# Optimization experiments

Hardware: AMD Instinct MI355X
Metric: run time of the kernel (lower is better)

Reference implementation:

```python
import jax, jax.numpy as jnp
import numpy as np

N_NODES = 50000

def setup_inputs() -> dict:
    key = jax.random.key(0)
    k1, k2, k3, k4, k5, k6 = jax.random.split(key, 6)
    T, D, N, E = 10000, 128, N_NODES, 800000
    impact = jax.random.normal(k1, (T, D), dtype=jnp.float32)
    W = jax.random.normal(k2, (D, D), dtype=jnp.float32)
    M = jax.random.normal(k3, (D, D), dtype=jnp.float32)
    node_ids = jax.random.randint(k4, (N,), 0, T, dtype=jnp.int64)
    neighbor_ids = jax.random.randint(k5, (E,), 0, T, dtype=jnp.int64)
    neighbor_segments = jnp.sort(jax.random.randint(k6, (E,), 0, N, dtype=jnp.int64))
    return {"impact": impact, "W": W, "M": M, "node_ids": node_ids,
            "neighbor_ids": neighbor_ids, "neighbor_segments": neighbor_segments}

def reference(impact, W, M, node_ids, neighbor_ids, neighbor_segments):
    # Per node i (type k_i): s_i = relu(W @ h[k_i] + sum_{j in N(i)} M @ h[type_j])
    # result = softmax(sum_i s_i) over the D feature axis.
    self_feats = impact[node_ids]                          # (N, D) gather
    neigh_feats = impact[neighbor_ids]                     # (E, D) gather
    neigh_sum = jax.ops.segment_sum(neigh_feats, neighbor_segments,
                                    num_segments=N_NODES)  # (N, D) scatter-add
    pre = self_feats @ W.T + neigh_sum @ M.T               # (N, D)
    result = jnp.sum(jax.nn.relu(pre), axis=0)             # (D,)
    return jax.nn.softmax(result, axis=0)
```

## Files before the change

### kernel.cpp

```cpp
#include <hip/hip_runtime.h>
#include <hip/hip_fp16.h>

#define DDIM 128
#define ACC_BLOCKS 2048
#define NWALK (ACC_BLOCKS * 4)
#define RED_BLOCKS 64

typedef unsigned int uint;
typedef unsigned short ushort;
typedef __attribute__((ext_vector_type(8))) short bf16x8;
typedef __attribute__((ext_vector_type(4))) float f32x4;

static __device__ __forceinline__ ushort f2bf(float x) {
    uint u = __float_as_uint(x);
    u += 0x7fffu + ((u >> 16) & 1u);
    return (ushort)(u >> 16);
}

static __device__ __forceinline__ bf16x8 load_frag8(const float* base) {
    const float4 p = *reinterpret_cast<const float4*>(base);
    const float4 q = *reinterpret_cast<const float4*>(base + 4);
    bf16x8 f;
    f[0] = (short)f2bf(p.x); f[1] = (short)f2bf(p.y);
    f[2] = (short)f2bf(p.z); f[3] = (short)f2bf(p.w);
    f[4] = (short)f2bf(q.x); f[5] = (short)f2bf(q.y);
    f[6] = (short)f2bf(q.z); f[7] = (short)f2bf(q.w);
    return f;
}

__global__ __launch_bounds__(256) void fat_prep_precompute(
    const float* __restrict__ impact,
    const float* __restrict__ W,
    const float* __restrict__ Mm,
    __half* __restrict__ WhH,
    __half* __restrict__ MhH,
    const int* __restrict__ segs,
    const int* __restrict__ node_ids,
    const int* __restrict__ neighbor_ids,
    int* __restrict__ items,
    int* __restrict__ wstart,
    int* __restrict__ done,
    int T, int N, int E, int PB, int whoff, int mhoff)
{
    if ((int)blockIdx.x >= PB) {
        const int x = ((int)blockIdx.x - PB) * 256 + (int)threadIdx.x;
        const int K = N + E;
        if (x == 0) *done = 0;

        if (x < E) {
            const int sc = segs[x];
            const int sp = (x == 0) ? -1 : segs[x - 1];
            const int sn = (x + 1 < E) ? segs[x + 1] : N;

            items[x + sc + 1] = (mhoff + neighbor_ids[x] * 256)
                              | ((sn != sc) ? (int)0x80000000 : 0);

            for (int i = sp + 1; i <= sc; ++i)
                items[x + i] = (whoff + node_ids[i] * 256)
                             | ((i < sc) ? (int)0x80000000 : 0);

            if (x == E - 1) {
                for (int i = sc + 1; i < N; ++i)
                    items[E + i] = (whoff + node_ids[i] * 256) | (int)0x80000000;
#pragma unroll
                for (int q = 0; q < 32; ++q) items[K + q] = whoff;
            }
        } else if (x <= E + NWALK) {
            const int w = x - E;
            int ws;
            if (w == 0) ws = 0;
            else {
                const long long t = (long long)w * E / NWALK;
                if (t >= E) ws = K;
                else {
                    const int n = segs[(int)t];
                    int lo = 0, hi = (int)t;
                    while (lo < hi) {
                        const int mid = (lo + hi) >> 1;
                        if (segs[mid] < n) lo = mid + 1; else hi = mid;
                    }
                    ws = lo + n;
                }
            }
            wstart[w] = ws;
        }
        return;
    }

    const int lane = threadIdx.x & 63;
    const int wv   = threadIdx.x >> 6;
    const int t0   = (int)blockIdx.x * 32;
    const int r16  = lane & 15;
    const int kg   = lane >> 4;

    bf16x8 A[2][4];
#pragma unroll
    for (int rt = 0; rt < 2; ++rt) {
        int t = t0 + rt * 16 + r16;
        if (t >= T) t = T - 1;
        const float* abase = impact + (size_t)t * DDIM + kg * 8;
#pragma unroll
        for (int k0i = 0; k0i < 4; ++k0i)
            A[rt][k0i] = load_frag8(abase + k0i * 32);
    }

#pragma unroll
    for (int dti = 0; dti < 2; ++dti) {
        const int d0 = (wv * 2 + dti) * 16;
#pragma unroll
        for (int m = 0; m < 2; ++m) {
            const float* mat = (m == 0) ? W : Mm;
            __half* out = (m == 0) ? WhH : MhH;
            const float* bbase = mat + (size_t)(d0 + r16) * DDIM + kg * 8;
            f32x4 acc0 = {0.f, 0.f, 0.f, 0.f};
            f32x4 acc1 = {0.f, 0.f, 0.f, 0.f};
#pragma unroll
            for (int k0i = 0; k0i < 4; ++k0i) {
                const bf16x8 b = load_frag8(bbase + k0i * 32);
                acc0 = __builtin_amdgcn_mfma_f32_16x16x32_bf16(A[0][k0i], b, acc0, 0, 0, 0);
                acc1 = __builtin_amdgcn_mfma_f32_16x16x32_bf16(A[1][k0i], b, acc1, 0, 0, 0);
            }
            const int dcol = d0 + r16;
#pragma unroll
            for (int r = 0; r < 4; ++r) {
                const int tr0 = t0 + kg * 4 + r;
                const int tr1 = tr0 + 16;
                if (tr0 < T) out[(size_t)tr0 * DDIM + dcol] = __float2half(acc0[r]);
                if (tr1 < T) out[(size_t)tr1 * DDIM + dcol] = __float2half(acc1[r]);
            }
        }
    }
}

__global__ __launch_bounds__(256, 8) void accumulate_items(
    const char* __restrict__ tab,
    const int* __restrict__ items,
    const int* __restrict__ wstart,
    float* __restrict__ partials)
{
    const int lane = threadIdx.x & 63;
    const int wv   = __builtin_amdgcn_readfirstlane(threadIdx.x >> 6);
    const int w    = blockIdx.x * 4 + wv;

    const uint lb = (uint)lane << 2;

    const __half2 zero2 = __floats2half2_rn(0.f, 0.f);
    __half2 cc = zero2;
    float a0 = 0.f, a1 = 0.f;

    int k = __builtin_amdgcn_readfirstlane(wstart[w]);
    const int kend = __builtin_amdgcn_readfirstlane(wstart[w + 1]);

#define GATH(IW) (*reinterpret_cast<const __half2*>(tab + (((uint)(IW)) & 0x7fffffffu) + lb))
#define ACC(IW, V) { \
    cc = __hadd2(cc, V); \
    if ((IW) < 0) { \
        const float2 f = __half22float2(cc); \
        a0 += fmaxf(f.x, 0.f); a1 += fmaxf(f.y, 0.f); \
        cc = zero2; \
    } }
#define LOADI(Pa, Pb, Pc, Pd, kk) { \
    Pa = *reinterpret_cast<const int4*>(items + (kk)); \
    Pb = *reinterpret_cast<const int4*>(items + (kk) + 4); \
    Pc = *reinterpret_cast<const int4*>(items + (kk) + 8); \
    Pd = *reinterpret_cast<const int4*>(items + (kk) + 12); }
#define GATHER16(V, Pa, Pb, Pc, Pd) { \
    V[0] = GATH(Pa.x);  V[1] = GATH(Pa.y);  V[2]  = GATH(Pa.z);  V[3]  = GATH(Pa.w); \
    V[4] = GATH(Pb.x);  V[5] = GATH(Pb.y);  V[6]  = GATH(Pb.z);  V[7]  = GATH(Pb.w); \
    V[8] = GATH(Pc.x);  V[9] = GATH(Pc.y);  V[10] = GATH(Pc.z);  V[11] = GATH(Pc.w); \
    V[12] = GATH(Pd.x); V[13] = GATH(Pd.y); V[14] = GATH(Pd.z);  V[15] = GATH(Pd.w); }
#define ACC16(V, Pa, Pb, Pc, Pd) { \
    ACC(Pa.x, V[0]);  ACC(Pa.y, V[1]);  ACC(Pa.z, V[2]);   ACC(Pa.w, V[3]); \
    ACC(Pb.x, V[4]);  ACC(Pb.y, V[5]);  ACC(Pb.z, V[6]);   ACC(Pb.w, V[7]); \
    ACC(Pc.x, V[8]);  ACC(Pc.y, V[9]);  ACC(Pc.z, V[10]);  ACC(Pc.w, V[11]); \
    ACC(Pd.x, V[12]); ACC(Pd.y, V[13]); ACC(Pd.z, V[14]);  ACC(Pd.w, V[15]); }

    while (k < kend && (k & 15)) {
        const int iw = items[k];
        const __half2 v = GATH(iw);
        ACC(iw, v);
        ++k;
    }

    if (k + 32 <= kend) {
        int4 Aa, Ab, Ac, Ad, Ba, Bb, Bc, Bd;
        __half2 u[16], v[16];
        LOADI(Aa, Ab, Ac, Ad, k);
        GATHER16(u, Aa, Ab, Ac, Ad);
        LOADI(Ba, Bb, Bc, Bd, k + 16);
        k += 32;
        for (;;) {
            GATHER16(v, Ba, Bb, Bc, Bd);
            ACC16(u, Aa, Ab, Ac, Ad);
            if (k + 16 <= kend) { LOADI(Aa, Ab, Ac, Ad, k); k += 16; }
            else { ACC16(v, Ba, Bb, Bc, Bd); break; }
            GATHER16(u, Aa, Ab, Ac, Ad);
            ACC16(v, Ba, Bb, Bc, Bd);
            if (k + 16 <= kend) { LOADI(Ba, Bb, Bc, Bd, k); k += 16; }
            else { ACC16(u, Aa, Ab, Ac, Ad); break; }
        }
    }
    while (k < kend) {
        const int iw = items[k];
        const __half2 v = GATH(iw);
        ACC(iw, v);
        ++k;
    }

    {
        const float2 f = __half22float2(cc);
        a0 += fmaxf(f.x, 0.f);
        a1 += fmaxf(f.y, 0.f);
    }

    __shared__ float red[4][DDIM];
    red[wv][lane * 2 + 0] = a0;
    red[wv][lane * 2 + 1] = a1;
    __syncthreads();
    const int tid = threadIdx.x;
    if (tid < DDIM) {
        partials[(size_t)blockIdx.x * DDIM + tid] =
            red[0][tid] + red[1][tid] + red[2][tid] + red[3][tid];
    }
}

__global__ __launch_bounds__(256) void reduce_softmax(
    const float* __restrict__ partials, float* __restrict__ out2,
    float* __restrict__ out, int* __restrict__ done, int nb)
{
    const int tid = threadIdx.x;
    const int d = tid & (DDIM - 1);
    const int h = tid >> 7;
    {
        const int rows = nb / RED_BLOCKS;
        const int r0 = blockIdx.x * rows;
        float s = 0.f;
        for (int r = r0 + h; r < r0 + rows; r += 2)
            s += partials[(size_t)r * DDIM + d];
        __shared__ float red[2][DDIM];
        red[h][d] = s;
        __syncthreads();
        if (tid < DDIM)
            out2[(size_t)blockIdx.x * DDIM + tid] = red[0][tid] + red[1][tid];
    }
    __threadfence();
    __shared__ int isLast;
    if (tid == 0) {
        const int v = atomicAdd(done, 1);
        isLast = (v == RED_BLOCKS - 1) ? 1 : 0;
    }
    __syncthreads();
    if (!isLast) return;
    __threadfence();

    float s = 0.f;
    for (int b = h; b < RED_BLOCKS; b += 2)
        s += out2[(size_t)b * DDIM + d];
    __shared__ float r2[2][DDIM];
    r2[h][d] = s;
    __syncthreads();

    __shared__ float vec[DDIM];
    __shared__ float tmp[DDIM];
    if (tid < DDIM) { const float v = r2[0][tid] + r2[1][tid]; vec[tid] = v; tmp[tid] = v; }
    __syncthreads();
    for (int o = 64; o > 0; o >>= 1) {
        if (tid < o) tmp[tid] = fmaxf(tmp[tid], tmp[tid + o]);
        __syncthreads();
    }
    const float mx = tmp[0];
    __syncthreads();
    float ev = 0.f;
    if (tid < DDIM) { ev = expf(vec[tid] - mx); tmp[tid] = ev; }
    __syncthreads();
    for (int o = 64; o > 0; o >>= 1) {
        if (tid < o) tmp[tid] += tmp[tid + o];
        __syncthreads();
    }
    if (tid < DDIM) out[tid] = ev / tmp[0];
}

extern "C" void kernel_launch(void* const* d_in, const int* in_sizes, int n_in,
                              void* d_out, int out_size, void* d_ws, size_t ws_size,
                              hipStream_t stream) {
    const float* impact        = (const float*)d_in[0];
    const float* W             = (const float*)d_in[1];
    const float* Mm            = (const float*)d_in[2];
    const int*   node_ids      = (const int*)d_in[3];
    const int*   neighbor_ids  = (const int*)d_in[4];
    const int*   neighbor_segs = (const int*)d_in[5];

    const int T = in_sizes[0] / DDIM;
    const int N = in_sizes[3];
    const int E = in_sizes[4];
    const int K = N + E;

    char* ws = (char*)d_ws;
    size_t off = 0;
    const int whoff = (int)off;
    __half* WhH = (__half*)(ws + off);  off += (size_t)T * DDIM * sizeof(__half);
    const int mhoff = (int)off;
    __half* MhH = (__half*)(ws + off);  off += (size_t)T * DDIM * sizeof(__half);
    float* partials = (float*)(ws + off); off += (size_t)ACC_BLOCKS * DDIM * sizeof(float);
    float* part2    = (float*)(ws + off); off += (size_t)RED_BLOCKS * DDIM * sizeof(float);
    int*   done     = (int*)(ws + off);   off += 256;
    off = (off + 255) & ~(size_t)255;
    int*   items    = (int*)(ws + off);   off += (size_t)(K + 32) * sizeof(int);
    int*   wstart   = (int*)(ws + off);   off += (size_t)(NWALK + 1) * sizeof(int);
    float* outf     = (float*)d_out;

    const int PB    = (T + 31) / 32;
    const int PREPB = (E + NWALK + 1 + 255) / 256;

    fat_prep_precompute<<<PB + PREPB, 256, 0, stream>>>(
        impact, W, Mm, WhH, MhH, neighbor_segs, node_ids, neighbor_ids,
        items, wstart, done, T, N, E, PB, whoff, mhoff);
    accumulate_items<<<ACC_BLOCKS, 256, 0, stream>>>(ws, items, wstart, partials);
    reduce_softmax<<<RED_BLOCKS, 256, 0, stream>>>(partials, part2, outf, done, ACC_BLOCKS);
}
```

Baseline: 57.30 us.

## Split each wavefront into two half-waves gathering two items per load

The accumulation kernel now has each half of a 64-lane wavefront gather a different item's 256-byte row, with each lane loading 8 bytes (4 halves) instead of 4 bytes. This doubles the bytes per lane per load and halves the number of gather instructions per item. Segment boundaries are handled by masked accumulation plus a cross-half shuffle at each flush. The cost is extra branching and shuffles whenever a pair contains a segment end, which happens often because segments average about 16 neighbours. The item padding grows to 64 entries to cover the wider loads.

```diff
diff --git a/kernel.cpp b/kernel.cpp
--- a/kernel.cpp
+++ b/kernel.cpp
@@ -15,6 +15,13 @@
     uint u = __float_as_uint(x);
     u += 0x7fffu + ((u >> 16) & 1u);
     return (ushort)(u >> 16);
+}
+
+static __device__ __forceinline__ __half2 u2h(uint u) {
+    union { uint a; __half2 b; } c; c.a = u; return c.b;
+}
+static __device__ __forceinline__ uint h2u(__half2 h) {
+    union { __half2 b; uint a; } c; c.b = h; return c.a;
 }
 
 static __device__ __forceinline__ bf16x8 load_frag8(const float* base) {
@@ -63,7 +70,7 @@
                 for (int i = sc + 1; i < N; ++i)
                     items[E + i] = (whoff + node_ids[i] * 256) | (int)0x80000000;
 #pragma unroll
-                for (int q = 0; q < 32; ++q) items[K + q] = whoff;
+                for (int q = 0; q < 64; ++q) items[K + q] = whoff;
             }
         } else if (x <= E + NWALK) {
             const int w = x - E;
@@ -71,7 +78,7 @@
             if (w == 0) ws = 0;
             else {
                 const long long t = (long long)w * E / NWALK;
-                if (t >= E) ws = K;
+                if (t >= E) ws = N + E;
                 else {
                     const int n = segs[(int)t];
                     int lo = 0, hi = (int)t;
@@ -132,92 +139,113 @@
     }
 }
 
-__global__ __launch_bounds__(256, 8) void accumulate_items(
+__global__ __launch_bounds__(256, 8) void accumulate_pairs(
     const char* __restrict__ tab,
     const int* __restrict__ items,
     const int* __restrict__ wstart,
     float* __restrict__ partials)
 {
-    const int lane = threadIdx.x & 63;
-    const int wv   = __builtin_amdgcn_readfirstlane(threadIdx.x >> 6);
+    const int tid  = threadIdx.x;
+    const int lane = tid & 63;
+    const int wv   = __builtin_amdgcn_readfirstlane(tid >> 6);
     const int w    = blockIdx.x * 4 + wv;
 
-    const uint lb = (uint)lane << 2;
+    const bool hiH = lane >= 32;
+    const uint lb  = (uint)(lane & 31) * 8u;
 
     const __half2 zero2 = __floats2half2_rn(0.f, 0.f);
-    __half2 cc = zero2;
-    float a0 = 0.f, a1 = 0.f;
+    __half2 c0 = zero2, c1 = zero2;
+    float a0 = 0.f, a1 = 0.f, a2 = 0.f, a3 = 0.f;
 
     int k = __builtin_amdgcn_readfirstlane(wstart[w]);
     const int kend = __builtin_amdgcn_readfirstlane(wstart[w + 1]);
 
-#define GATH(IW) (*reinterpret_cast<const __half2*>(tab + (((uint)(IW)) & 0x7fffffffu) + lb))
-#define ACC(IW, V) { \
-    cc = __hadd2(cc, V); \
-    if ((IW) < 0) { \
-        const float2 f = __half22float2(cc); \
-        a0 += fmaxf(f.x, 0.f); a1 += fmaxf(f.y, 0.f); \
-        cc = zero2; \
+#define FLUSH() { \
+    const __half2 s0f = u2h((uint)__shfl_xor((int)h2u(c0), 32, 64)); \
+    const __half2 s1f = u2h((uint)__shfl_xor((int)h2u(c1), 32, 64)); \
+    const float2 f0f = __half22float2(__hadd2(c0, s0f)); \
+    const float2 f1f = __half22float2(__hadd2(c1, s1f)); \
+    a0 += fmaxf(f0f.x, 0.f); a1 += fmaxf(f0f.y, 0.f); \
+    a2 += fmaxf(f1f.x, 0.f); a3 += fmaxf(f1f.y, 0.f); \
+    c0 = zero2; c1 = zero2; }
+
+#define SINGLE(IW) { \
+    const uint2 V = *reinterpret_cast<const uint2*>(tab + (((uint)(IW)) & 0x7fffffffu) + lb); \
+    c0 = hiH ? c0 : __hadd2(c0, u2h(V.x)); \
+    c1 = hiH ? c1 : __hadd2(c1, u2h(V.y)); \
+    if ((IW) < 0) FLUSH(); }
+
+#define GPAIR(V, S0, S1) { \
+    const uint o_ = ((uint)(hiH ? (S1) : (S0)) & 0x7fffffffu) + lb; \
+    V = *reinterpret_cast<const uint2*>(tab + o_); }
+
+#define APAIR(V, S0, S1) { \
+    if ((((S0) | (S1)) & (int)0x80000000) == 0) { \
+        c0 = __hadd2(c0, u2h(V.x)); c1 = __hadd2(c1, u2h(V.y)); \
+    } else { \
+        c0 = hiH ? c0 : __hadd2(c0, u2h(V.x)); \
+        c1 = hiH ? c1 : __hadd2(c1, u2h(V.y)); \
+        if ((S0) < 0) FLUSH(); \
+        c0 = hiH ? __hadd2(c0, u2h(V.x)) : c0; \
+        c1 = hiH ? __hadd2(c1, u2h(V.y)) : c1; \
+        if ((S1) < 0) FLUSH(); \
     } }
-#define LOADI(Pa, Pb, Pc, Pd, kk) { \
-    Pa = *reinterpret_cast<const int4*>(items + (kk)); \
-    Pb = *reinterpret_cast<const int4*>(items + (kk) + 4); \
-    Pc = *reinterpret_cast<const int4*>(items + (kk) + 8); \
-    Pd = *reinterpret_cast<const int4*>(items + (kk) + 12); }
-#define GATHER16(V, Pa, Pb, Pc, Pd) { \
-    V[0] = GATH(Pa.x);  V[1] = GATH(Pa.y);  V[2]  = GATH(Pa.z);  V[3]  = GATH(Pa.w); \
-    V[4] = GATH(Pb.x);  V[5] = GATH(Pb.y);  V[6]  = GATH(Pb.z);  V[7]  = GATH(Pb.w); \
-    V[8] = GATH(Pc.x);  V[9] = GATH(Pc.y);  V[10] = GATH(Pc.z);  V[11] = GATH(Pc.w); \
-    V[12] = GATH(Pd.x); V[13] = GATH(Pd.y); V[14] = GATH(Pd.z);  V[15] = GATH(Pd.w); }
-#define ACC16(V, Pa, Pb, Pc, Pd) { \
-    ACC(Pa.x, V[0]);  ACC(Pa.y, V[1]);  ACC(Pa.z, V[2]);   ACC(Pa.w, V[3]); \
-    ACC(Pb.x, V[4]);  ACC(Pb.y, V[5]);  ACC(Pb.z, V[6]);   ACC(Pb.w, V[7]); \
-    ACC(Pc.x, V[8]);  ACC(Pc.y, V[9]);  ACC(Pc.z, V[10]);  ACC(Pc.w, V[11]); \
-    ACC(Pd.x, V[12]); ACC(Pd.y, V[13]); ACC(Pd.z, V[14]);  ACC(Pd.w, V[15]); }
-
-    while (k < kend && (k & 15)) {
+
+#define LOAD8(I0, I1, kk) { \
+    I0 = *reinterpret_cast<const int4*>(items + (kk)); \
+    I1 = *reinterpret_cast<const int4*>(items + (kk) + 4); }
+#define G4(V, I0, I1) { \
+    GPAIR(V[0], I0.x, I0.y); GPAIR(V[1], I0.z, I0.w); \
+    GPAIR(V[2], I1.x, I1.y); GPAIR(V[3], I1.z, I1.w); }
+#define A4(V, I0, I1) { \
+    APAIR(V[0], I0.x, I0.y); APAIR(V[1], I0.z, I0.w); \
+    APAIR(V[2], I1.x, I1.y); APAIR(V[3], I1.z, I1.w); }
+
+    while (k < kend && (k & 3)) {
         const int iw = items[k];
-        const __half2 v = GATH(iw);
-        ACC(iw, v);
+        SINGLE(iw);
         ++k;
     }
 
-    if (k + 32 <= kend) {
-        int4 Aa, Ab, Ac, Ad, Ba, Bb, Bc, Bd;
-        __half2 u[16], v[16];
-        LOADI(Aa, Ab, Ac, Ad, k);
-        GATHER16(u, Aa, Ab, Ac, Ad);
-        LOADI(Ba, Bb, Bc, Bd, k + 16);
-        k += 32;
+    if (k + 16 <= kend) {
+        int4 Ia0, Ia1, Ib0, Ib1;
+        uint2 u[4], v[4];
+        LOAD8(Ia0, Ia1, k);
+        G4(u, Ia0, Ia1);
+        LOAD8(Ib0, Ib1, k + 8);
+        k += 16;
         for (;;) {
-            GATHER16(v, Ba, Bb, Bc, Bd);
-            ACC16(u, Aa, Ab, Ac, Ad);
-            if (k + 16 <= kend) { LOADI(Aa, Ab, Ac, Ad, k); k += 16; }
-            else { ACC16(v, Ba, Bb, Bc, Bd); break; }
-            GATHER16(u, Aa, Ab, Ac, Ad);
-            ACC16(v, Ba, Bb, Bc, Bd);
-            if (k + 16 <= kend) { LOADI(Ba, Bb, Bc, Bd, k); k += 16; }
-            else { ACC16(u, Aa, Ab, Ac, Ad); break; }
+            G4(v, Ib0, Ib1);
+            A4(u, Ia0, Ia1);
+            if (k + 8 <= kend) { LOAD8(Ia0, Ia1, k); k += 8; }
+            else { A4(v, Ib0, Ib1); break; }
+            G4(u, Ia0, Ia1);
+            A4(v, Ib0, Ib1);
+            if (k + 8 <= kend) { LOAD8(Ib0, Ib1, k); k += 8; }
+            else { A4(u, Ia0, Ia1); break; }
         }
+    }
+    while (k + 8 <= kend) {
+        int4 Ic0, Ic1;
+        uint2 t4[4];
+        LOAD8(Ic0, Ic1, k);
+        G4(t4, Ic0, Ic1);
+        A4(t4, Ic0, Ic1);
+        k += 8;
     }
     while (k < kend) {
         const int iw = items[k];
-        const __half2 v = GATH(iw);
-        ACC(iw, v);
+        SINGLE(iw);
         ++k;
     }
 
-    {
-        const float2 f = __half22float2(cc);
-        a0 += fmaxf(f.x, 0.f);
-        a1 += fmaxf(f.y, 0.f);
-    }
+    FLUSH();
 
     __shared__ float red[4][DDIM];
-    red[wv][lane * 2 + 0] = a0;
-    red[wv][lane * 2 + 1] = a1;
-    __syncthreads();
-    const int tid = threadIdx.x;
+    if (!hiH)
+        *reinterpret_cast<float4*>(&red[wv][(lane & 31) * 4]) =
+            make_float4(a0, a1, a2, a3);
+    __syncthreads();
     if (tid < DDIM) {
         partials[(size_t)blockIdx.x * DDIM + tid] =
             red[0][tid] + red[1][tid] + red[2][tid] + red[3][tid];
@@ -305,7 +333,7 @@
     float* part2    = (float*)(ws + off); off += (size_t)RED_BLOCKS * DDIM * sizeof(float);
     int*   done     = (int*)(ws + off);   off += 256;
     off = (off + 255) & ~(size_t)255;
-    int*   items    = (int*)(ws + off);   off += (size_t)(K + 32) * sizeof(int);
+    int*   items    = (int*)(ws + off);   off += (size_t)(K + 64) * sizeof(int);
     int*   wstart   = (int*)(ws + off);   off += (size_t)(NWALK + 1) * sizeof(int);
     float* outf     = (float*)d_out;
 
@@ -315,6 +343,6 @@
     fat_prep_precompute<<<PB + PREPB, 256, 0, stream>>>(
         impact, W, Mm, WhH, MhH, neighbor_segs, node_ids, neighbor_ids,
         items, wstart, done, T, N, E, PB, whoff, mhoff);
-    accumulate_items<<<ACC_BLOCKS, 256, 0, stream>>>(ws, items, wstart, partials);
+    accumulate_pairs<<<ACC_BLOCKS, 256, 0, stream>>>(ws, items, wstart, partials);
     reduce_softmax<<<RED_BLOCKS, 256, 0, stream>>>(partials, part2, outf, done, ACC_BLOCKS);
 }
```

New measurement: 61.42 us. +7.2%, slower.

## Gather rows with 16-byte loads by splitting each wavefront into four item streams

Applied to the files above, without the earlier changes.

The accumulation kernel now has each wavefront walk four independent item ranges at once. Each 16-lane quarter gathers a full 256-byte half-precision row using 16-byte loads, where before all 64 lanes each did a 4-byte load per item. Out-of-range slots are padded to point at a zero row, so ranges can be processed in aligned groups of four without tail loops. The change also halves the number of accumulate blocks and drops occupancy to 4 waves, and adds extra select and predication work on segment boundaries.

```diff
diff --git a/kernel.cpp b/kernel.cpp
--- a/kernel.cpp
+++ b/kernel.cpp
@@ -2,8 +2,8 @@
 #include <hip/hip_fp16.h>
 
 #define DDIM 128
-#define ACC_BLOCKS 2048
-#define NWALK (ACC_BLOCKS * 4)
+#define ACC_BLOCKS 1024
+#define NQUART (ACC_BLOCKS * 4 * 4)
 #define RED_BLOCKS 64
 
 typedef unsigned int uint;
@@ -15,6 +15,9 @@
     uint u = __float_as_uint(x);
     u += 0x7fffu + ((u >> 16) & 1u);
     return (ushort)(u >> 16);
+}
+static __device__ __forceinline__ __half2 u2h(uint u) {
+    union { uint a; __half2 b; } c; c.a = u; return c.b;
 }
 
 static __device__ __forceinline__ bf16x8 load_frag8(const float* base) {
@@ -40,12 +43,14 @@
     int* __restrict__ items,
     int* __restrict__ wstart,
     int* __restrict__ done,
-    int T, int N, int E, int PB, int whoff, int mhoff)
+    uint* __restrict__ zrow,
+    int T, int N, int E, int PB, int whoff, int mhoff, int zpad)
 {
     if ((int)blockIdx.x >= PB) {
         const int x = ((int)blockIdx.x - PB) * 256 + (int)threadIdx.x;
         const int K = N + E;
         if (x == 0) *done = 0;
+        if (x < 64) zrow[x] = 0u;
 
         if (x < E) {
             const int sc = segs[x];
@@ -63,15 +68,15 @@
                 for (int i = sc + 1; i < N; ++i)
                     items[E + i] = (whoff + node_ids[i] * 256) | (int)0x80000000;
 #pragma unroll
-                for (int q = 0; q < 32; ++q) items[K + q] = whoff;
+                for (int q = 0; q < 64; ++q) items[K + q] = zpad;
             }
-        } else if (x <= E + NWALK) {
+        } else if (x <= E + NQUART) {
             const int w = x - E;
             int ws;
             if (w == 0) ws = 0;
             else {
-                const long long t = (long long)w * E / NWALK;
-                if (t >= E) ws = K;
+                const long long t = (long long)w * E / NQUART;
+                if (t >= E) ws = N + E;
                 else {
                     const int n = segs[(int)t];
                     int lo = 0, hi = (int)t;
@@ -132,95 +137,125 @@
     }
 }
 
-__global__ __launch_bounds__(256, 8) void accumulate_items(
+__global__ __launch_bounds__(256, 4) void accumulate_quads(
     const char* __restrict__ tab,
     const int* __restrict__ items,
-    const int* __restrict__ wstart,
-    float* __restrict__ partials)
+    const int* __restrict__ qstart,
+    float* __restrict__ partials,
+    int zpad)
 {
-    const int lane = threadIdx.x & 63;
-    const int wv   = __builtin_amdgcn_readfirstlane(threadIdx.x >> 6);
-    const int w    = blockIdx.x * 4 + wv;
-
-    const uint lb = (uint)lane << 2;
-
-    const __half2 zero2 = __floats2half2_rn(0.f, 0.f);
-    __half2 cc = zero2;
-    float a0 = 0.f, a1 = 0.f;
-
-    int k = __builtin_amdgcn_readfirstlane(wstart[w]);
-    const int kend = __builtin_amdgcn_readfirstlane(wstart[w + 1]);
-
-#define GATH(IW) (*reinterpret_cast<const __half2*>(tab + (((uint)(IW)) & 0x7fffffffu) + lb))
-#define ACC(IW, V) { \
-    cc = __hadd2(cc, V); \
-    if ((IW) < 0) { \
-        const float2 f = __half22float2(cc); \
-        a0 += fmaxf(f.x, 0.f); a1 += fmaxf(f.y, 0.f); \
-        cc = zero2; \
+    const int tid  = threadIdx.x;
+    const int lane = tid & 63;
+    const int wv   = __builtin_amdgcn_readfirstlane(tid >> 6);
+    const int qb   = (blockIdx.x * 4 + wv) * 4;
+
+    const int l0 = __builtin_amdgcn_readfirstlane(qstart[qb + 0]);
+    const int l1 = __builtin_amdgcn_readfirstlane(qstart[qb + 1]);
+    const int l2 = __builtin_amdgcn_readfirstlane(qstart[qb + 2]);
+    const int l3 = __builtin_amdgcn_readfirstlane(qstart[qb + 3]);
+    const int e0 = l1, e1 = l2, e2 = l3;
+    const int e3 = __builtin_amdgcn_readfirstlane(qstart[qb + 4]);
+    int k0 = l0 & ~3, k1 = l1 & ~3, k2 = l2 & ~3, k3 = l3 & ~3;
+
+    const int  qid  = lane >> 4;
+    const bool b0   = (qid & 1) != 0;
+    const bool b1   = (qid & 2) != 0;
+    const uint qoff = (uint)(lane & 15) * 16u;
+
+    const __half2 z2 = __floats2half2_rn(0.f, 0.f);
+    __half2 c0 = z2, c1 = z2, c2 = z2, c3 = z2;
+    float a0 = 0.f, a1 = 0.f, a2 = 0.f, a3 = 0.f;
+    float a4 = 0.f, a5 = 0.f, a6 = 0.f, a7 = 0.f;
+
+#define GETJ(S, j) ((j) == 0 ? (S).x : (j) == 1 ? (S).y : (j) == 2 ? (S).z : (S).w)
+
+#define LDW4(Wd, kk, lo, ke) { \
+    const int4 raw_ = *reinterpret_cast<const int4*>(items + (kk)); \
+    Wd.x = ((kk) + 0 >= (lo) && (kk) + 0 < (ke)) ? raw_.x : zpad; \
+    Wd.y = ((kk) + 1 >= (lo) && (kk) + 1 < (ke)) ? raw_.y : zpad; \
+    Wd.z = ((kk) + 2 >= (lo) && (kk) + 2 < (ke)) ? raw_.z : zpad; \
+    Wd.w = ((kk) + 3 >= (lo) && (kk) + 3 < (ke)) ? raw_.w : zpad; }
+
+#define LOADB(WA, WB, WC, WD) { \
+    LDW4(WA, k0, l0, e0); LDW4(WB, k1, l1, e1); \
+    LDW4(WC, k2, l2, e2); LDW4(WD, k3, l3, e3); \
+    k0 = min(k0 + 4, (e0 + 3) & ~3); k1 = min(k1 + 4, (e1 + 3) & ~3); \
+    k2 = min(k2 + 4, (e2 + 3) & ~3); k3 = min(k3 + 4, (e3 + 3) & ~3); }
+
+#define GATHERB(V, WA, WB, WC, WD) { \
+    _Pragma("unroll") \
+    for (int j = 0; j < 4; ++j) { \
+        const int wa_ = GETJ(WA, j), wb_ = GETJ(WB, j); \
+        const int wc_ = GETJ(WC, j), wd_ = GETJ(WD, j); \
+        const int s01_ = b0 ? wb_ : wa_; \
+        const int s23_ = b0 ? wd_ : wc_; \
+        const int sel_ = b1 ? s23_ : s01_; \
+        V[j] = *reinterpret_cast<const uint4*>(tab + (((uint)sel_ & 0x7fffffffu) + qoff)); \
     } }
-#define LOADI(Pa, Pb, Pc, Pd, kk) { \
-    Pa = *reinterpret_cast<const int4*>(items + (kk)); \
-    Pb = *reinterpret_cast<const int4*>(items + (kk) + 4); \
-    Pc = *reinterpret_cast<const int4*>(items + (kk) + 8); \
-    Pd = *reinterpret_cast<const int4*>(items + (kk) + 12); }
-#define GATHER16(V, Pa, Pb, Pc, Pd) { \
-    V[0] = GATH(Pa.x);  V[1] = GATH(Pa.y);  V[2]  = GATH(Pa.z);  V[3]  = GATH(Pa.w); \
-    V[4] = GATH(Pb.x);  V[5] = GATH(Pb.y);  V[6]  = GATH(Pb.z);  V[7]  = GATH(Pb.w); \
-    V[8] = GATH(Pc.x);  V[9] = GATH(Pc.y);  V[10] = GATH(Pc.z);  V[11] = GATH(Pc.w); \
-    V[12] = GATH(Pd.x); V[13] = GATH(Pd.y); V[14] = GATH(Pd.z);  V[15] = GATH(Pd.w); }
-#define ACC16(V, Pa, Pb, Pc, Pd) { \
-    ACC(Pa.x, V[0]);  ACC(Pa.y, V[1]);  ACC(Pa.z, V[2]);   ACC(Pa.w, V[3]); \
-    ACC(Pb.x, V[4]);  ACC(Pb.y, V[5]);  ACC(Pb.z, V[6]);   ACC(Pb.w, V[7]); \
-    ACC(Pc.x, V[8]);  ACC(Pc.y, V[9]);  ACC(Pc.z, V[10]);  ACC(Pc.w, V[11]); \
-    ACC(Pd.x, V[12]); ACC(Pd.y, V[13]); ACC(Pd.z, V[14]);  ACC(Pd.w, V[15]); }
-
-    while (k < kend && (k & 15)) {
-        const int iw = items[k];
-        const __half2 v = GATH(iw);
-        ACC(iw, v);
-        ++k;
-    }
-
-    if (k + 32 <= kend) {
-        int4 Aa, Ab, Ac, Ad, Ba, Bb, Bc, Bd;
-        __half2 u[16], v[16];
-        LOADI(Aa, Ab, Ac, Ad, k);
-        GATHER16(u, Aa, Ab, Ac, Ad);
-        LOADI(Ba, Bb, Bc, Bd, k + 16);
-        k += 32;
+
+#define PROCB(V, WA, WB, WC, WD) { \
+    _Pragma("unroll") \
+    for (int j = 0; j < 4; ++j) { \
+        const int wa_ = GETJ(WA, j), wb_ = GETJ(WB, j); \
+        const int wc_ = GETJ(WC, j), wd_ = GETJ(WD, j); \
+        c0 = __hadd2(c0, u2h(V[j].x)); \
+        c1 = __hadd2(c1, u2h(V[j].y)); \
+        c2 = __hadd2(c2, u2h(V[j].z)); \
+        c3 = __hadd2(c3, u2h(V[j].w)); \
+        if ((wa_ | wb_ | wc_ | wd_) < 0) { \
+            const int s01_ = b0 ? wb_ : wa_; \
+            const int s23_ = b0 ? wd_ : wc_; \
+            const bool fm_ = (b1 ? s23_ : s01_) < 0; \
+            float2 f_; \
+            f_ = __half22float2(c0); \
+            a0 += fm_ ? fmaxf(f_.x, 0.f) : 0.f;  a1 += fm_ ? fmaxf(f_.y, 0.f) : 0.f; \
+            f_ = __half22float2(c1); \
+            a2 += fm_ ? fmaxf(f_.x, 0.f) : 0.f;  a3 += fm_ ? fmaxf(f_.y, 0.f) : 0.f; \
+            f_ = __half22float2(c2); \
+            a4 += fm_ ? fmaxf(f_.x, 0.f) : 0.f;  a5 += fm_ ? fmaxf(f_.y, 0.f) : 0.f; \
+            f_ = __half22float2(c3); \
+            a6 += fm_ ? fmaxf(f_.x, 0.f) : 0.f;  a7 += fm_ ? fmaxf(f_.y, 0.f) : 0.f; \
+            c0 = fm_ ? z2 : c0;  c1 = fm_ ? z2 : c1; \
+            c2 = fm_ ? z2 : c2;  c3 = fm_ ? z2 : c3; \
+        } \
+    } }
+
+    bool more = (k0 < e0) || (k1 < e1) || (k2 < e2) || (k3 < e3);
+    if (more) {
+        int4 WA, WB, WC, WD, XA, XB, XC, XD;
+        uint4 V[4], U[4];
+        LOADB(WA, WB, WC, WD);
+        GATHERB(V, WA, WB, WC, WD);
         for (;;) {
-            GATHER16(v, Ba, Bb, Bc, Bd);
-            ACC16(u, Aa, Ab, Ac, Ad);
-            if (k + 16 <= kend) { LOADI(Aa, Ab, Ac, Ad, k); k += 16; }
-            else { ACC16(v, Ba, Bb, Bc, Bd); break; }
-            GATHER16(u, Aa, Ab, Ac, Ad);
-            ACC16(v, Ba, Bb, Bc, Bd);
-            if (k + 16 <= kend) { LOADI(Ba, Bb, Bc, Bd, k); k += 16; }
-            else { ACC16(u, Aa, Ab, Ac, Ad); break; }
+            const bool m2 = (k0 < e0) || (k1 < e1) || (k2 < e2) || (k3 < e3);
+            if (m2) { LOADB(XA, XB, XC, XD); GATHERB(U, XA, XB, XC, XD); }
+            PROCB(V, WA, WB, WC, WD);
+            if (!m2) break;
+            const bool m3 = (k0 < e0) || (k1 < e1) || (k2 < e2) || (k3 < e3);
+            if (m3) { LOADB(WA, WB, WC, WD); GATHERB(V, WA, WB, WC, WD); }
+            PROCB(U, XA, XB, XC, XD);
+            if (!m3) break;
         }
     }
-    while (k < kend) {
-        const int iw = items[k];
-        const __half2 v = GATH(iw);
-        ACC(iw, v);
-        ++k;
-    }
 
     {
-        const float2 f = __half22float2(cc);
-        a0 += fmaxf(f.x, 0.f);
-        a1 += fmaxf(f.y, 0.f);
-    }
-
-    __shared__ float red[4][DDIM];
-    red[wv][lane * 2 + 0] = a0;
-    red[wv][lane * 2 + 1] = a1;
-    __syncthreads();
-    const int tid = threadIdx.x;
+        float2 f;
+        f = __half22float2(c0); a0 += fmaxf(f.x, 0.f); a1 += fmaxf(f.y, 0.f);
+        f = __half22float2(c1); a2 += fmaxf(f.x, 0.f); a3 += fmaxf(f.y, 0.f);
+        f = __half22float2(c2); a4 += fmaxf(f.x, 0.f); a5 += fmaxf(f.y, 0.f);
+        f = __half22float2(c3); a6 += fmaxf(f.x, 0.f); a7 += fmaxf(f.y, 0.f);
+    }
+
+    __shared__ float red[4][4][DDIM];
+    const int fl = lane & 15;
+    *reinterpret_cast<float4*>(&red[wv][qid][fl * 8 + 0]) = make_float4(a0, a1, a2, a3);
+    *reinterpret_cast<float4*>(&red[wv][qid][fl * 8 + 4]) = make_float4(a4, a5, a6, a7);
+    __syncthreads();
     if (tid < DDIM) {
-        partials[(size_t)blockIdx.x * DDIM + tid] =
-            red[0][tid] + red[1][tid] + red[2][tid] + red[3][tid];
+        float s = 0.f;
+#pragma unroll
+        for (int g = 0; g < 16; ++g) s += red[g >> 2][g & 3][tid];
+        partials[(size_t)blockIdx.x * DDIM + tid] = s;
     }
 }
 
@@ -301,20 +336,22 @@
     __half* WhH = (__half*)(ws + off);  off += (size_t)T * DDIM * sizeof(__half);
     const int mhoff = (int)off;
     __half* MhH = (__half*)(ws + off);  off += (size_t)T * DDIM * sizeof(__half);
+    const int zoff = (int)off;
+    uint* zrow = (uint*)(ws + off);     off += 64 * sizeof(uint);
     float* partials = (float*)(ws + off); off += (size_t)ACC_BLOCKS * DDIM * sizeof(float);
     float* part2    = (float*)(ws + off); off += (size_t)RED_BLOCKS * DDIM * sizeof(float);
     int*   done     = (int*)(ws + off);   off += 256;
     off = (off + 255) & ~(size_t)255;
-    int*   items    = (int*)(ws + off);   off += (size_t)(K + 32) * sizeof(int);
-    int*   wstart   = (int*)(ws + off);   off += (size_t)(NWALK + 1) * sizeof(int);
+    int*   items    = (int*)(ws + off);   off += (size_t)(K + 64) * sizeof(int);
+    int*   wstart   = (int*)(ws + off);   off += (size_t)(NQUART + 1) * sizeof(int);
     float* outf     = (float*)d_out;
 
     const int PB    = (T + 31) / 32;
-    const int PREPB = (E + NWALK + 1 + 255) / 256;
+    const int PREPB = (E + NQUART + 1 + 255) / 256;
 
     fat_prep_precompute<<<PB + PREPB, 256, 0, stream>>>(
         impact, W, Mm, WhH, MhH, neighbor_segs, node_ids, neighbor_ids,
-        items, wstart, done, T, N, E, PB, whoff, mhoff);
-    accumulate_items<<<ACC_BLOCKS, 256, 0, stream>>>(ws, items, wstart, partials);
+        items, wstart, done, zrow, T, N, E, PB, whoff, mhoff, zoff);
+    accumulate_quads<<<ACC_BLOCKS, 256, 0, stream>>>(ws, items, wstart, partials, zoff);
     reduce_softmax<<<RED_BLOCKS, 256, 0, stream>>>(partials, part2, outf, done, ACC_BLOCKS);
 }
```

After: 72.41 us. +26.4%, slower.
